# Kernel optimization log

Hardware: AMD Instinct MI355X
Metric: run time of the kernel (lower is better)

Reference implementation:

```python
import jax, jax.numpy as jnp
import numpy as np

B, S, D = 4, 8192, 512
H, DK = 8, 64
LOCAL_W = 256
GLOBAL_STRIDE = 64
LN_EPS = 1e-5


def setup_inputs() -> dict:
    key = jax.random.key(0)
    ks = jax.random.split(key, 9)
    scale = 1.0 / np.sqrt(D)
    def lin(k, din, dout):
        return jax.random.normal(k, (din, dout), jnp.float32) * scale
    return {
        "x": jax.random.normal(ks[0], (B, S, D), jnp.float32),
        "lq_w": lin(ks[1], D, D), "lq_b": jnp.zeros((D,), jnp.float32),
        "lk_w": lin(ks[2], D, D), "lk_b": jnp.zeros((D,), jnp.float32),
        "lv_w": lin(ks[3], D, D), "lv_b": jnp.zeros((D,), jnp.float32),
        "gq_w": lin(ks[4], D, D), "gq_b": jnp.zeros((D,), jnp.float32),
        "gk_w": lin(ks[5], D, D), "gk_b": jnp.zeros((D,), jnp.float32),
        "gv_w": lin(ks[6], D, D), "gv_b": jnp.zeros((D,), jnp.float32),
        "out_w": jax.random.normal(ks[7], (2 * D, D), jnp.float32) * (1.0 / np.sqrt(2 * D)),
        "out_b": jnp.zeros((D,), jnp.float32),
        "ln_g": jnp.ones((D,), jnp.float32),
        "ln_b": jnp.zeros((D,), jnp.float32),
    }


def _local_attention(x, qw, qb, kw, kb, vw, vb):
    # x: [B,S,D]; S divisible by LOCAL_W -> no padding path.
    nW = S // LOCAL_W
    xw = x.reshape(B, nW, LOCAL_W, D)
    def heads(w, b):
        y = jnp.einsum('bnwd,de->bnwe', xw, w) + b  # [B,nW,W,D]
        return y.reshape(B, nW, LOCAL_W, H, DK).transpose(0, 1, 3, 2, 4)  # [B,nW,H,W,dk]
    q, k, v = heads(qw, qb), heads(kw, kb), heads(vw, vb)
    scores = jnp.einsum('bnhqd,bnhkd->bnhqk', q, k) / np.sqrt(DK)
    attn = jax.nn.softmax(scores, axis=-1)
    out = jnp.einsum('bnhqk,bnhkd->bnhqd', attn, v)  # [B,nW,H,W,dk]
    return out.transpose(0, 1, 3, 2, 4).reshape(B, S, D)


def _global_attention(x, qw, qb, kw, kb, vw, vb):
    gc = x[:, ::GLOBAL_STRIDE]                       # [B,G,D]
    G = gc.shape[1]
    q = (x @ qw + qb).reshape(B, S, H, DK)           # [B,S,H,dk]
    k = (gc @ kw + kb).reshape(B, G, H, DK)
    v = (gc @ vw + vb).reshape(B, G, H, DK)
    scores = jnp.einsum('bshd,bghd->bhsg', q, k) / np.sqrt(DK)
    attn = jax.nn.softmax(scores, axis=-1)
    out = jnp.einsum('bhsg,bghd->bshd', attn, v)
    return out.reshape(B, S, D)


def reference(x, lq_w, lq_b, lk_w, lk_b, lv_w, lv_b,
              gq_w, gq_b, gk_w, gk_b, gv_w, gv_b,
              out_w, out_b, ln_g, ln_b):
    local = _local_attention(x, lq_w, lq_b, lk_w, lk_b, lv_w, lv_b)
    glob = _global_attention(x, gq_w, gq_b, gk_w, gk_b, gv_w, gv_b)
    combined = jnp.concatenate([local, glob], axis=-1) @ out_w + out_b
    h = x + combined  # dropout is identity in eval
    mu = jnp.mean(h, axis=-1, keepdims=True)
    var = jnp.var(h, axis=-1, keepdims=True)
    return (h - mu) / jnp.sqrt(var + LN_EPS) * ln_g + ln_b
```

## Files before the change

### kernel.cpp

```cpp
#include <hip/hip_runtime.h>
#include <hip/hip_bf16.h>
#include <stdint.h>

#define B_ 4
#define S_ 8192
#define D_ 512
#define H_ 8
#define DK_ 64
#define G_ 128
#define ROWS_ (B_*S_)

typedef unsigned short u16;
typedef __attribute__((ext_vector_type(8))) short short8;
typedef __attribute__((ext_vector_type(4))) short short4v;
typedef __attribute__((ext_vector_type(4))) float floatx4;

static __device__ __forceinline__ float bf2f(u16 u){
  union { uint32_t i; float f; } v; v.i = ((uint32_t)u) << 16; return v.f;
}
static __device__ __forceinline__ u16 f2bf(float f){
  union { float f; uint32_t i; } v; v.f = f;
  uint32_t u = v.i; u += 0x7fff + ((u >> 16) & 1); return (u16)(u >> 16);
}

static __device__ __forceinline__ void glds16(const u16* g, u16* l){
  __builtin_amdgcn_global_load_lds(
      (const __attribute__((address_space(1))) void*)g,
      (__attribute__((address_space(3))) void*)l, 16, 0, 0);
}

__global__ void cast_x_kernel(const float* __restrict__ x, u16* __restrict__ xb, int n4){
  int i = blockIdx.x*blockDim.x + threadIdx.x;
  if (i >= n4) return;
  float4 v = ((const float4*)x)[i];
  short4v o;
  o[0] = (short)f2bf(v.x); o[1] = (short)f2bf(v.y);
  o[2] = (short)f2bf(v.z); o[3] = (short)f2bf(v.w);
  *(short4v*)(xb + (size_t)i*4) = o;
}

__global__ void transpose_cast_kernel(const float* __restrict__ W, u16* __restrict__ Ot, int K, int N){
  __shared__ float t[64][65];
  int n0 = blockIdx.x*64, k0 = blockIdx.y*64;
  int tx = threadIdx.x & 63, ty = threadIdx.x >> 6;
#pragma unroll
  for (int j=0;j<16;j++){ int k = ty + j*4; t[k][tx] = W[(size_t)(k0+k)*N + n0+tx]; }
  __syncthreads();
#pragma unroll
  for (int j=0;j<16;j++){ int n = ty + j*4; Ot[(size_t)(n0+n)*K + k0 + tx] = f2bf(t[tx][n]); }
}

__global__ void build_bias_kernel(float* __restrict__ bcat, float* __restrict__ bg,
    const float* lq_b, const float* lk_b, const float* lv_b, const float* gq_b,
    const float* gk_b, const float* gv_b){
  int i = blockIdx.x*blockDim.x + threadIdx.x;
  if (i < 2048){
    const float* s = (i < 512) ? lq_b : (i < 1024) ? lk_b : (i < 1536) ? lv_b : gq_b;
    bcat[i] = s[i & 511];
  } else if (i < 3072){
    int j = i - 2048;
    bg[j] = (j < 512) ? gk_b[j] : gv_b[j - 512];
  }
}

__global__ void gather_xg_kernel(const u16* __restrict__ xb, u16* __restrict__ xg){
  int t = blockIdx.x*blockDim.x + threadIdx.x;
  int row = t >> 6;
  int c8 = (t & 63) * 8;
  int b = row >> 7, g = row & 127;
  const u16* src = xb + ((size_t)(b*S_ + g*64))*D_ + c8;
  u16* dst = xg + (size_t)row*D_ + c8;
  *(short8*)dst = *(const short8*)src;
}

template<int EPI>
__global__ __launch_bounds__(512, 1) void gemm_big(
    const u16* __restrict__ A, const u16* __restrict__ Bt,
    const float* __restrict__ bias, void* __restrict__ Cv,
    const float* __restrict__ X, int M, int N, int K)
{
  __shared__ u16 SM[4][16384];
  const int tid = threadIdx.x, lane = tid & 63, w = tid >> 6;
  const int wm = w >> 2, wn = w & 3;
  const int gx = gridDim.x;
  const int h = blockIdx.y * gx + blockIdx.x;
  const int chunk = (gx * gridDim.y) >> 3;
  const int work = (h & 7) * chunk + (h >> 3);
  const int bx = work % gx, by = work / gx;
  const int m0 = by*256, n0 = bx*256;
  const int T = K >> 5;

  const u16* gsrc[4]; int loff[4];
#pragma unroll
  for (int j = 0; j < 4; j++){
    int fb  = w*4 + j;
    int isB = fb >> 4;
    int blk = fb & 15;
    const u16* bp = isB ? Bt : A;
    int row = (isB ? n0 : m0) + blk*16 + (lane & 15);
    gsrc[j] = bp + (size_t)row * K + ((lane >> 4) * 8);
    loff[j] = fb*512;
  }

  floatx4 acc[8][4] = {};

#pragma unroll
  for (int tt = 0; tt < 3; tt++)
#pragma unroll
    for (int j = 0; j < 4; j++)
      glds16(gsrc[j] + tt*32, &SM[tt][loff[j]]);

#pragma unroll 4
  for (int t = 0; t < T; t++){
    if (t <= T - 3)      asm volatile("s_waitcnt vmcnt(8)" ::: "memory");
    else if (t == T - 2) asm volatile("s_waitcnt vmcnt(4)" ::: "memory");
    else                 asm volatile("s_waitcnt vmcnt(0)" ::: "memory");
    __builtin_amdgcn_s_barrier();

    if (t + 3 < T){
      u16* Sb = &SM[(t + 3) & 3][0];
#pragma unroll
      for (int j = 0; j < 4; j++) glds16(gsrc[j] + (t+3)*32, Sb + loff[j]);
    }

    const u16* Tb = &SM[t & 3][0];
    short8 aR[8], bR[4];
#pragma unroll
    for (int i=0;i<8;i++) aR[i] = *(const short8*)(Tb + (wm*8 + i)*512 + lane*8);
#pragma unroll
    for (int j=0;j<4;j++) bR[j] = *(const short8*)(Tb + (16 + wn*4 + j)*512 + lane*8);
#pragma unroll
    for (int i=0;i<8;i++)
#pragma unroll
      for (int j=0;j<4;j++)
        acc[i][j] = __builtin_amdgcn_mfma_f32_16x16x32_bf16(aR[i], bR[j], acc[i][j], 0,0,0);
  }

#pragma unroll
  for (int mi=0; mi<8; mi++)
#pragma unroll
    for (int nj=0; nj<4; nj++){
      int col = n0 + (wn*4 + nj)*16 + (lane & 15);
      float bv = bias[col];
#pragma unroll
      for (int ii=0; ii<4; ii++){
        size_t row = (size_t)(m0 + (wm*8 + mi)*16 + (lane>>4)*4 + ii);
        float v = acc[mi][nj][ii] + bv;
        if (EPI == 0){
          ((u16*)Cv)[row*N + col] = f2bf(v);
        } else {
          ((float*)Cv)[row*N + col] = v + X[row*N + col];
        }
      }
    }
}

__global__ __launch_bounds__(256) void gemm_small(
    const u16* __restrict__ A, const u16* __restrict__ Bt,
    const float* __restrict__ bias, u16* __restrict__ C,
    int M, int N, int K)
{
  __shared__ u16 As[128*32];
  __shared__ u16 Bs[128*32];
  const int tid = threadIdx.x, lane = tid & 63, w = tid >> 6;
  const int m0 = blockIdx.y*128, n0 = blockIdx.x*128;
  const int wm = (w>>1)*64, wn = (w&1)*64;
  floatx4 acc[4][4] = {};
  const int c0 = 2*w;
  const int sr = lane >> 2;
  const int sc = (lane & 3) * 8;
  const u16* ga0 = A  + (size_t)(m0 +  c0     *16 + sr)*K + sc;
  const u16* ga1 = A  + (size_t)(m0 + (c0 + 1)*16 + sr)*K + sc;
  const u16* gb0 = Bt + (size_t)(n0 +  c0     *16 + sr)*K + sc;
  const u16* gb1 = Bt + (size_t)(n0 + (c0 + 1)*16 + sr)*K + sc;
  u16* la0 = &As[ c0     *512];
  u16* la1 = &As[(c0 + 1)*512];
  u16* lb0 = &Bs[ c0     *512];
  u16* lb1 = &Bs[(c0 + 1)*512];

  for (int k0 = 0; k0 < K; k0 += 32){
    __syncthreads();
    glds16(ga0 + k0, la0);
    glds16(ga1 + k0, la1);
    glds16(gb0 + k0, lb0);
    glds16(gb1 + k0, lb1);
    __syncthreads();
    short8 af[4], bf[4];
#pragma unroll
    for (int i=0;i<4;i++) af[i] = *(const short8*)&As[(wm + i*16 + (lane&15))*32 + (lane>>4)*8];
#pragma unroll
    for (int i=0;i<4;i++) bf[i] = *(const short8*)&Bs[(wn + i*16 + (lane&15))*32 + (lane>>4)*8];
#pragma unroll
    for (int mi=0;mi<4;mi++)
#pragma unroll
      for (int ni=0;ni<4;ni++)
        acc[mi][ni] = __builtin_amdgcn_mfma_f32_16x16x32_bf16(af[mi], bf[ni], acc[mi][ni], 0,0,0);
  }

#pragma unroll
  for (int mi=0;mi<4;mi++)
#pragma unroll
    for (int ni=0;ni<4;ni++){
      int col = n0 + wn + ni*16 + (lane&15);
      float bv = bias[col];
#pragma unroll
      for (int i=0;i<4;i++){
        size_t row = (size_t)(m0 + wm + mi*16 + (lane>>4)*4 + i);
        C[row*N + col] = f2bf(acc[mi][ni][i] + bv);
      }
    }
}

template<int KVLEN, int KSTRIDE, bool GLOBAL>
__global__ __launch_bounds__(512, 2) void attn_kernel(
    const u16* __restrict__ qkv, const u16* __restrict__ kvbuf, u16* __restrict__ comb)
{
  __shared__ u16 SM[KVLEN*256];
  u16* Kl = SM;
  u16* Vt = SM + KVLEN*64;
  u16* Pl = SM + KVLEN*128;
  const int tid = threadIdx.x, lane = tid & 63, w = tid >> 6;
  const int h = blockIdx.x, n = blockIdx.y, b = blockIdx.z;
  const size_t qrow0 = (size_t)b*S_ + (size_t)n*256;
  const int krow0 = GLOBAL ? b*G_ : (b*S_ + n*256);
  const int qc = (GLOBAL ? 1536 : 0)   + h*DK_;
  const int kc = (GLOBAL ? 0    : 512) + h*DK_;
  const int vc = (GLOBAL ? 512  : 1024)+ h*DK_;
  const int oc = (GLOBAL ? 512  : 0)   + h*DK_;
  constexpr int NF = KVLEN/16;

  {
    const int rpw = KVLEN/8;
    const int r0w = w * rpw;
    const int cg = ((lane & 7) ^ (lane >> 3)) * 8;
    const int rl = lane >> 3;
#pragma unroll
    for (int j = 0; j < rpw; j += 8){
      int row = r0w + j + rl;
      glds16(kvbuf + (size_t)(krow0 + row)*KSTRIDE + kc + cg, &Kl[(r0w + j)*64]);
    }
  }
  if (tid < KVLEN){
    const int r0 = (tid >> 3) * 8;
    const int c0 = (tid & 7) * 8;
    const u16* vp = kvbuf + (size_t)(krow0 + r0)*KSTRIDE + vc + c0;
    short8 rIn[8];
#pragma unroll
    for (int i=0;i<8;i++) rIn[i] = *(const short8*)(vp + (size_t)i*KSTRIDE);
#pragma unroll
    for (int i=0;i<8;i++){
      short8 o;
#pragma unroll
      for (int j=0;j<8;j++) o[j] = rIn[j][i];
      int d = c0 + i;
      *(short8*)&Vt[d*KVLEN + ((((r0>>3) ^ (d&7))) << 3)] = o;
    }
  }
  __syncthreads();

  const float scale = 0.125f;
  const int Pbase = w*16*KVLEN;

  for (int sp = 2*w; sp < 2*w + 2; sp++){
    const u16* qp = qkv + (qrow0 + sp*16 + (lane&15))*2048 + qc + ((lane>>4)*8);
    short8 qf0 = *(const short8*)qp;
    short8 qf1 = *(const short8*)(qp + 32);

    floatx4 sacc[NF];
#pragma unroll
    for (int nf = 0; nf < NF; nf++){
      const u16* kb = &Kl[(nf*16 + (lane&15))*64];
      short8 kf0 = *(const short8*)(kb + ((( lane>>4)      ^ (lane&7)) << 3));
      short8 kf1 = *(const short8*)(kb + ((((lane>>4) + 4) ^ (lane&7)) << 3));
      floatx4 z = {0.f,0.f,0.f,0.f};
      z = __builtin_amdgcn_mfma_f32_16x16x32_bf16(qf0, kf0, z, 0,0,0);
      z = __builtin_amdgcn_mfma_f32_16x16x32_bf16(qf1, kf1, z, 0,0,0);
      sacc[nf] = z;
    }

    float mx[4] = {-1e30f,-1e30f,-1e30f,-1e30f};
#pragma unroll
    for (int nf=0;nf<NF;nf++)
#pragma unroll
      for (int i=0;i<4;i++) mx[i] = fmaxf(mx[i], sacc[nf][i]);
#pragma unroll
    for (int i=0;i<4;i++){
#pragma unroll
      for (int msk=1; msk<16; msk<<=1) mx[i] = fmaxf(mx[i], __shfl_xor(mx[i], msk));
    }
    float sm[4] = {0.f,0.f,0.f,0.f};
#pragma unroll
    for (int nf=0;nf<NF;nf++)
#pragma unroll
      for (int i=0;i<4;i++){
        float e = __expf((sacc[nf][i] - mx[i]) * scale);
        sacc[nf][i] = e; sm[i] += e;
      }
#pragma unroll
    for (int i=0;i<4;i++){
#pragma unroll
      for (int msk=1; msk<16; msk<<=1) sm[i] += __shfl_xor(sm[i], msk);
      sm[i] = 1.f / sm[i];
    }

#pragma unroll
    for (int nf=0;nf<NF;nf++)
#pragma unroll
      for (int i=0;i<4;i++){
        int row = (lane>>4)*4 + i;
        int ch  = nf*2 + ((lane>>3)&1);
        Pl[Pbase + row*KVLEN + ((ch ^ (row&7)) << 3) + (lane&7)] = f2bf(sacc[nf][i]*sm[i]);
      }

    floatx4 oacc[4] = {};
#pragma unroll
    for (int kk=0; kk<KVLEN/32; kk++){
      int prow = lane & 15;
      short8 pf = *(const short8*)&Pl[Pbase + prow*KVLEN + (((kk*4 + (lane>>4)) ^ (prow&7)) << 3)];
#pragma unroll
      for (int nd=0; nd<4; nd++){
        int d = nd*16 + (lane&15);
        short8 vf = *(const short8*)&Vt[d*KVLEN + (((kk*4 + (lane>>4)) ^ (d&7)) << 3)];
        oacc[nd] = __builtin_amdgcn_mfma_f32_16x16x32_bf16(pf, vf, oacc[nd], 0,0,0);
      }
    }

#pragma unroll
    for (int nd=0; nd<4; nd++)
#pragma unroll
      for (int i=0;i<4;i++){
        size_t row = qrow0 + sp*16 + (lane>>4)*4 + i;
        comb[row*1024 + oc + nd*16 + (lane&15)] = f2bf(oacc[nd][i]);
      }
  }
}

__global__ __launch_bounds__(256) void ln_kernel(float* __restrict__ out,
    const float* __restrict__ g, const float* __restrict__ bta){
  int lane = threadIdx.x & 63, w = threadIdx.x >> 6;
  size_t row = (size_t)blockIdx.x*4 + w;
  float* p = out + row*D_;
  float4 v0 = ((float4*)p)[lane];
  float4 v1 = ((float4*)p)[64 + lane];
  float s = v0.x+v0.y+v0.z+v0.w + v1.x+v1.y+v1.z+v1.w;
  float q = v0.x*v0.x+v0.y*v0.y+v0.z*v0.z+v0.w*v0.w
          + v1.x*v1.x+v1.y*v1.y+v1.z*v1.z+v1.w*v1.w;
#pragma unroll
  for (int msk=1; msk<64; msk<<=1){ s += __shfl_xor(s, msk); q += __shfl_xor(q, msk); }
  float mean = s * (1.f/512.f);
  float var  = q * (1.f/512.f) - mean*mean;
  float inv  = rsqrtf(var + 1e-5f);
  float4 g0 = ((const float4*)g)[lane],  g1 = ((const float4*)g)[64 + lane];
  float4 b0 = ((const float4*)bta)[lane], b1 = ((const float4*)bta)[64 + lane];
  v0.x = (v0.x-mean)*inv*g0.x + b0.x; v0.y = (v0.y-mean)*inv*g0.y + b0.y;
  v0.z = (v0.z-mean)*inv*g0.z + b0.z; v0.w = (v0.w-mean)*inv*g0.w + b0.w;
  v1.x = (v1.x-mean)*inv*g1.x + b1.x; v1.y = (v1.y-mean)*inv*g1.y + b1.y;
  v1.z = (v1.z-mean)*inv*g1.z + b1.z; v1.w = (v1.w-mean)*inv*g1.w + b1.w;
  ((float4*)p)[lane] = v0;
  ((float4*)p)[64 + lane] = v1;
}

extern "C" void kernel_launch(void* const* d_in, const int* in_sizes, int n_in,
                              void* d_out, int out_size, void* d_ws, size_t ws_size,
                              hipStream_t stream)
{
  const float* x    = (const float*)d_in[0];
  const float* lq_w = (const float*)d_in[1];
  const float* lq_b = (const float*)d_in[2];
  const float* lk_w = (const float*)d_in[3];
  const float* lk_b = (const float*)d_in[4];
  const float* lv_w = (const float*)d_in[5];
  const float* lv_b = (const float*)d_in[6];
  const float* gq_w = (const float*)d_in[7];
  const float* gq_b = (const float*)d_in[8];
  const float* gk_w = (const float*)d_in[9];
  const float* gk_b = (const float*)d_in[10];
  const float* gv_w = (const float*)d_in[11];
  const float* gv_b = (const float*)d_in[12];
  const float* out_w = (const float*)d_in[13];
  const float* out_b = (const float*)d_in[14];
  const float* ln_g = (const float*)d_in[15];
  const float* ln_b = (const float*)d_in[16];

  char* ws = (char*)d_ws;
  size_t off = 0;
  auto alloc = [&](size_t bytes)->void*{ void* p = ws + off; off += (bytes + 255) & ~255ULL; return p; };
  u16*  xb    = (u16*) alloc((size_t)ROWS_*D_*2);
  u16*  xg    = (u16*) alloc((size_t)512*512*2);
  u16*  WcatT = (u16*) alloc((size_t)2048*512*2);
  u16*  WgT   = (u16*) alloc((size_t)1024*512*2);
  u16*  WoutT = (u16*) alloc((size_t)512*1024*2);
  float* bcat = (float*)alloc(2048*4);
  float* bg   = (float*)alloc(1024*4);
  u16*  qkvg  = (u16*) alloc((size_t)ROWS_*2048*2);
  u16*  gkv   = (u16*) alloc((size_t)512*1024*2);
  u16*  comb  = (u16*) alloc((size_t)ROWS_*1024*2);

  cast_x_kernel<<<16384,256,0,stream>>>(x, xb, ROWS_*D_/4);
  transpose_cast_kernel<<<dim3(8,8),256,0,stream>>>(lq_w, WcatT + (size_t)0*512*512, 512, 512);
  transpose_cast_kernel<<<dim3(8,8),256,0,stream>>>(lk_w, WcatT + (size_t)1*512*512, 512, 512);
  transpose_cast_kernel<<<dim3(8,8),256,0,stream>>>(lv_w, WcatT + (size_t)2*512*512, 512, 512);
  transpose_cast_kernel<<<dim3(8,8),256,0,stream>>>(gq_w, WcatT + (size_t)3*512*512, 512, 512);
  transpose_cast_kernel<<<dim3(8,8),256,0,stream>>>(gk_w, WgT, 512, 512);
  transpose_cast_kernel<<<dim3(8,8),256,0,stream>>>(gv_w, WgT + (size_t)512*512, 512, 512);
  transpose_cast_kernel<<<dim3(8,16),256,0,stream>>>(out_w, WoutT, 1024, 512);
  build_bias_kernel<<<12,256,0,stream>>>(bcat, bg, lq_b, lk_b, lv_b, gq_b, gk_b, gv_b);
  gather_xg_kernel<<<128,256,0,stream>>>(xb, xg);

  gemm_big<0><<<dim3(8,128),512,0,stream>>>(xb, WcatT, bcat, qkvg, nullptr, ROWS_, 2048, 512);
  gemm_small<<<dim3(8,4),256,0,stream>>>(xg, WgT, bg, gkv, 512, 1024, 512);

  attn_kernel<256,2048,false><<<dim3(8,32,4),512,0,stream>>>(qkvg, qkvg, comb);
  attn_kernel<128,1024,true ><<<dim3(8,32,4),512,0,stream>>>(qkvg, gkv,  comb);

  gemm_big<1><<<dim3(2,128),512,0,stream>>>(comb, WoutT, out_b, d_out, x, ROWS_, 512, 1024);
  ln_kernel<<<8192,256,0,stream>>>((float*)d_out, ln_g, ln_b);
}
```

Baseline: 327.0 us.

## Double-buffer gemm_big LDS, write bf16 residual sum, read it in layernorm

The main GEMM drops from a 4-stage to a 2-stage LDS pipeline (64KB instead of 128KB shared memory) and its launch bounds change from 1 to 4 blocks per CU. The aim is to let several blocks share a CU, with an extra barrier per iteration protecting buffer reuse. The output GEMM now adds the residual from the bf16 copy of x and writes a bf16 intermediate into the reused qkvg buffer, so it no longer reads fp32 x or writes fp32 output. Layernorm reads that bf16 buffer and writes fp32 once, which cuts memory traffic but rounds the pre-norm sum to bf16, costing some precision.

```diff
diff --git a/kernel.cpp b/kernel.cpp
--- a/kernel.cpp
+++ b/kernel.cpp
@@ -74,12 +74,12 @@
 }
 
 template<int EPI>
-__global__ __launch_bounds__(512, 1) void gemm_big(
+__global__ __launch_bounds__(512, 4) void gemm_big(
     const u16* __restrict__ A, const u16* __restrict__ Bt,
-    const float* __restrict__ bias, void* __restrict__ Cv,
-    const float* __restrict__ X, int M, int N, int K)
+    const float* __restrict__ bias, u16* __restrict__ C,
+    const u16* __restrict__ X, int M, int N, int K)
 {
-  __shared__ u16 SM[4][16384];
+  __shared__ u16 SM[2][16384];
   const int tid = threadIdx.x, lane = tid & 63, w = tid >> 6;
   const int wm = w >> 2, wn = w & 3;
   const int gx = gridDim.x;
@@ -105,25 +105,21 @@
   floatx4 acc[8][4] = {};
 
 #pragma unroll
-  for (int tt = 0; tt < 3; tt++)
-#pragma unroll
-    for (int j = 0; j < 4; j++)
-      glds16(gsrc[j] + tt*32, &SM[tt][loff[j]]);
-
-#pragma unroll 4
+  for (int j = 0; j < 4; j++) glds16(gsrc[j], &SM[0][loff[j]]);
+
+#pragma unroll 2
   for (int t = 0; t < T; t++){
-    if (t <= T - 3)      asm volatile("s_waitcnt vmcnt(8)" ::: "memory");
-    else if (t == T - 2) asm volatile("s_waitcnt vmcnt(4)" ::: "memory");
-    else                 asm volatile("s_waitcnt vmcnt(0)" ::: "memory");
+    if (t + 1 < T){
+      u16* Sb = &SM[(t + 1) & 1][0];
+#pragma unroll
+      for (int j = 0; j < 4; j++) glds16(gsrc[j] + (t+1)*32, Sb + loff[j]);
+      asm volatile("s_waitcnt vmcnt(4)" ::: "memory");
+    } else {
+      asm volatile("s_waitcnt vmcnt(0)" ::: "memory");
+    }
     __builtin_amdgcn_s_barrier();
 
-    if (t + 3 < T){
-      u16* Sb = &SM[(t + 3) & 3][0];
-#pragma unroll
-      for (int j = 0; j < 4; j++) glds16(gsrc[j] + (t+3)*32, Sb + loff[j]);
-    }
-
-    const u16* Tb = &SM[t & 3][0];
+    const u16* Tb = &SM[t & 1][0];
     short8 aR[8], bR[4];
 #pragma unroll
     for (int i=0;i<8;i++) aR[i] = *(const short8*)(Tb + (wm*8 + i)*512 + lane*8);
@@ -134,6 +130,7 @@
 #pragma unroll
       for (int j=0;j<4;j++)
         acc[i][j] = __builtin_amdgcn_mfma_f32_16x16x32_bf16(aR[i], bR[j], acc[i][j], 0,0,0);
+    __builtin_amdgcn_s_barrier();
   }
 
 #pragma unroll
@@ -146,11 +143,8 @@
       for (int ii=0; ii<4; ii++){
         size_t row = (size_t)(m0 + (wm*8 + mi)*16 + (lane>>4)*4 + ii);
         float v = acc[mi][nj][ii] + bv;
-        if (EPI == 0){
-          ((u16*)Cv)[row*N + col] = f2bf(v);
-        } else {
-          ((float*)Cv)[row*N + col] = v + X[row*N + col];
-        }
+        if (EPI == 1) v += bf2f(X[row*N + col]);
+        C[row*N + col] = f2bf(v);
       }
     }
 }
@@ -335,29 +329,30 @@
   }
 }
 
-__global__ __launch_bounds__(256) void ln_kernel(float* __restrict__ out,
-    const float* __restrict__ g, const float* __restrict__ bta){
+__global__ __launch_bounds__(256) void ln_kernel(const u16* __restrict__ hb,
+    float* __restrict__ out, const float* __restrict__ g, const float* __restrict__ bta){
   int lane = threadIdx.x & 63, w = threadIdx.x >> 6;
   size_t row = (size_t)blockIdx.x*4 + w;
-  float* p = out + row*D_;
-  float4 v0 = ((float4*)p)[lane];
-  float4 v1 = ((float4*)p)[64 + lane];
-  float s = v0.x+v0.y+v0.z+v0.w + v1.x+v1.y+v1.z+v1.w;
-  float q = v0.x*v0.x+v0.y*v0.y+v0.z*v0.z+v0.w*v0.w
-          + v1.x*v1.x+v1.y*v1.y+v1.z*v1.z+v1.w*v1.w;
+  const u16* p = hb + row*D_;
+  short8 hv = *(const short8*)(p + lane*8);
+  float f[8]; float s = 0.f, q = 0.f;
+#pragma unroll
+  for (int i=0;i<8;i++){ f[i] = bf2f((u16)hv[i]); s += f[i]; q += f[i]*f[i]; }
 #pragma unroll
   for (int msk=1; msk<64; msk<<=1){ s += __shfl_xor(s, msk); q += __shfl_xor(q, msk); }
   float mean = s * (1.f/512.f);
   float var  = q * (1.f/512.f) - mean*mean;
   float inv  = rsqrtf(var + 1e-5f);
-  float4 g0 = ((const float4*)g)[lane],  g1 = ((const float4*)g)[64 + lane];
-  float4 b0 = ((const float4*)bta)[lane], b1 = ((const float4*)bta)[64 + lane];
-  v0.x = (v0.x-mean)*inv*g0.x + b0.x; v0.y = (v0.y-mean)*inv*g0.y + b0.y;
-  v0.z = (v0.z-mean)*inv*g0.z + b0.z; v0.w = (v0.w-mean)*inv*g0.w + b0.w;
-  v1.x = (v1.x-mean)*inv*g1.x + b1.x; v1.y = (v1.y-mean)*inv*g1.y + b1.y;
-  v1.z = (v1.z-mean)*inv*g1.z + b1.z; v1.w = (v1.w-mean)*inv*g1.w + b1.w;
-  ((float4*)p)[lane] = v0;
-  ((float4*)p)[64 + lane] = v1;
+  float4 g0 = ((const float4*)g)[lane*2],   g1 = ((const float4*)g)[lane*2+1];
+  float4 b0 = ((const float4*)bta)[lane*2], b1 = ((const float4*)bta)[lane*2+1];
+  float4 o0, o1;
+  o0.x = (f[0]-mean)*inv*g0.x + b0.x; o0.y = (f[1]-mean)*inv*g0.y + b0.y;
+  o0.z = (f[2]-mean)*inv*g0.z + b0.z; o0.w = (f[3]-mean)*inv*g0.w + b0.w;
+  o1.x = (f[4]-mean)*inv*g1.x + b1.x; o1.y = (f[5]-mean)*inv*g1.y + b1.y;
+  o1.z = (f[6]-mean)*inv*g1.z + b1.z; o1.w = (f[7]-mean)*inv*g1.w + b1.w;
+  float* op = out + row*D_;
+  ((float4*)op)[lane*2]     = o0;
+  ((float4*)op)[lane*2 + 1] = o1;
 }
 
 extern "C" void kernel_launch(void* const* d_in, const int* in_sizes, int n_in,
@@ -395,6 +390,7 @@
   u16*  qkvg  = (u16*) alloc((size_t)ROWS_*2048*2);
   u16*  gkv   = (u16*) alloc((size_t)512*1024*2);
   u16*  comb  = (u16*) alloc((size_t)ROWS_*1024*2);
+  u16*  hbuf  = qkvg;
 
   cast_x_kernel<<<16384,256,0,stream>>>(x, xb, ROWS_*D_/4);
   transpose_cast_kernel<<<dim3(8,8),256,0,stream>>>(lq_w, WcatT + (size_t)0*512*512, 512, 512);
@@ -413,6 +409,6 @@
   attn_kernel<256,2048,false><<<dim3(8,32,4),512,0,stream>>>(qkvg, qkvg, comb);
   attn_kernel<128,1024,true ><<<dim3(8,32,4),512,0,stream>>>(qkvg, gkv,  comb);
 
-  gemm_big<1><<<dim3(2,128),512,0,stream>>>(comb, WoutT, out_b, d_out, x, ROWS_, 512, 1024);
-  ln_kernel<<<8192,256,0,stream>>>((float*)d_out, ln_g, ln_b);
-}
+  gemm_big<1><<<dim3(2,128),512,0,stream>>>(comb, WoutT, out_b, hbuf, xb, ROWS_, 512, 1024);
+  ln_kernel<<<8192,256,0,stream>>>(hbuf, (float*)d_out, ln_g, ln_b);
+}
```

Measured after the change: 942.3 us. 2.88x slower.
